# Optimization experiments

Hardware: AMD Instinct MI355X
Metric: run time of the kernel (lower is better)

The kernel has to match this reference:

```python
import jax, jax.numpy as jnp
import numpy as np

K, T, D, S, A, C, H = 128, 64, 128, 512, 4, 16, 512
N_LEAVES = 128
TEMP = 1.0          # sample_merge_temp
EPS_SQRT = 1e-4     # distances.EPSILON ** 0.5 with EPSILON = 1e-8
_SQ_EPS = 1e-12     # numerical guard inside sqrt (diagonal of pairwise dists is 0)


def setup_inputs() -> dict:
    key = jax.random.key(0)
    ks = jax.random.split(key, 11)
    leaf_counts_Kxt = jax.random.randint(ks[0], (K, T), 1, 5)
    embeddings_KxtxD = jax.random.normal(ks[1], (K, T, D), jnp.float32)
    log_felsensteins_KxtxSxA = jax.random.normal(ks[2], (K, T, S, A), jnp.float32)
    site_positions_SxC = jax.random.uniform(ks[3], (S, C), jnp.float32)
    W1 = jax.random.normal(ks[4], (2 * D, H), jnp.float32) / jnp.sqrt(2.0 * D)
    b1 = jnp.zeros((H,), jnp.float32)
    W2 = jax.random.normal(ks[5], (H, D), jnp.float32) / jnp.sqrt(1.0 * H)
    b2 = jnp.zeros((D,), jnp.float32)
    gumbel_Kxtt = jax.random.gumbel(ks[6], (K, T * T), jnp.float32)
    u1_K = jax.random.uniform(ks[7], (K,), jnp.float32, minval=1e-6, maxval=1.0)
    u2_K = jax.random.uniform(ks[8], (K,), jnp.float32, minval=1e-6, maxval=1.0)
    return {
        "N": N_LEAVES,
        "leaf_counts_Kxt": leaf_counts_Kxt,
        "embeddings_KxtxD": embeddings_KxtxD,
        "log_felsensteins_KxtxSxA": log_felsensteins_KxtxSxA,
        "site_positions_SxC": site_positions_SxC,
        "W1": W1, "b1": b1, "W2": W2, "b2": b2,
        "gumbel_Kxtt": gumbel_Kxtt, "u1_K": u1_K, "u2_K": u2_K,
    }


def _merge_encoder(c1_KxD, c2_KxD, W1, b1, W2, b2):
    # MLP merge encoder: MLP(concat(child1, child2)) -> parent embedding
    h = jax.nn.relu(jnp.concatenate([c1_KxD, c2_KxD], axis=-1) @ W1 + b1)
    return h @ W2 + b2


def reference(N, leaf_counts_Kxt, embeddings_KxtxD, log_felsensteins_KxtxSxA,
              site_positions_SxC, W1, b1, W2, b2, gumbel_Kxtt, u1_K, u2_K):
    Kp, t = leaf_counts_Kxt.shape
    ar = jnp.arange(Kp)

    # --- pairwise distances over all t*t subtree pairs per particle ---
    diff_Kxtxtxd = embeddings_KxtxD[:, :, None, :] - embeddings_KxtxD[:, None, :, :]
    pd_Kxtxt = jnp.sqrt(jnp.sum(diff_Kxtxtxd * diff_Kxtxtxd, axis=-1) + _SQ_EPS)
    merge_log_weights_Kxtxt = -pd_Kxtxt / TEMP
    # diagonal_scatter(-inf): forbid self-merges
    eye = jnp.eye(t, dtype=bool)[None]
    merge_log_weights_Kxtxt = jnp.where(eye, -jnp.inf, merge_log_weights_Kxtxt)

    # --- categorical merge sampling (gumbel-max with pre-drawn noise) ---
    flat_Kxtt = merge_log_weights_Kxtxt.reshape(Kp, t * t)
    sample_K = jnp.argmax(flat_Kxtt + gumbel_Kxtt, axis=1)
    idx1_K = sample_K // t
    idx2_K = sample_K % t
    log_merge_prob_K = (flat_Kxtt[ar, sample_K] + jnp.log(2.0)
                        - jax.scipy.special.logsumexp(flat_Kxtt, axis=1))

    # --- merged embedding ---
    child1_KxD = embeddings_KxtxD[ar, idx1_K]
    child2_KxD = embeddings_KxtxD[ar, idx2_K]
    embedding_KxD = _merge_encoder(child1_KxD, child2_KxD, W1, b1, W2, b2)

    # --- branch lengths sampled from Exp(rate = 1/(dist + eps)) ---
    d1_K = jnp.sqrt(jnp.sum((child1_KxD - embedding_KxD) ** 2, axis=-1) + _SQ_EPS)
    d2_K = jnp.sqrt(jnp.sum((child2_KxD - embedding_KxD) ** 2, axis=-1) + _SQ_EPS)
    rate1_K = 1.0 / (d1_K + EPS_SQRT)
    rate2_K = 1.0 / (d2_K + EPS_SQRT)
    branch1_K = -(1.0 / rate1_K) * jnp.log(u1_K)
    branch2_K = -(1.0 / rate2_K) * jnp.log(u2_K)
    log_branch1_prior_K = jnp.log(rate1_K) - rate1_K * branch1_K
    log_branch2_prior_K = jnp.log(rate2_K) - rate2_K * branch2_K

    log_v_plus_K = log_merge_prob_K + log_branch1_prior_K + log_branch2_prior_K

    # --- over-counting correction ---
    ones_K = jnp.sum(leaf_counts_Kxt == 1, axis=1)
    ones_K = ones_K - (leaf_counts_Kxt[ar, idx1_K] == 1).astype(ones_K.dtype)
    ones_K = ones_K - (leaf_counts_Kxt[ar, idx2_K] == 1).astype(ones_K.dtype)
    log_v_minus_K = jnp.log((N - ones_K).astype(jnp.float32))

    return (idx1_K, idx2_K, branch1_K, branch2_K, embedding_KxD,
            log_v_plus_K, log_v_minus_K)
```

## Files before the change

kernel.cpp:

```cpp
#include <hip/hip_runtime.h>
#include <math.h>

#define Kp 128
#define Tn 64
#define Dn 128
#define Hn 512
#define RS 136

typedef __attribute__((ext_vector_type(8))) short short8;
typedef __attribute__((ext_vector_type(4))) float f32x4;

__device__ __forceinline__ float bfpair(unsigned int hi_bits, unsigned int lo_bits) {
    return __uint_as_float(hi_bits) + __uint_as_float(lo_bits);
}

__global__ __launch_bounds__(512, 1) void ep_kernel(
    const int*   __restrict__ Nptr,
    const int*   __restrict__ leaf,
    const float* __restrict__ emb,
    const float* __restrict__ W1,
    const float* __restrict__ b1,
    const float* __restrict__ W2,
    const float* __restrict__ b2,
    const float* __restrict__ gum,
    const float* __restrict__ u1,
    const float* __restrict__ u2,
    float* __restrict__ out)
{
    const int k    = blockIdx.x;
    const int tid  = threadIdx.x;
    const int lane = tid & 63;
    const int wid  = tid >> 6;

    __shared__ unsigned short EH[Tn * RS];
    __shared__ unsigned short EL[Tn * RS];
    __shared__ float hsh[Hn];
    __shared__ float buf[2112];
    __shared__ float nI[Tn];
    __shared__ float sBest[8]; __shared__ int sIdx[8]; __shared__ float sW[8];
    __shared__ float sSum[8];
    __shared__ float sD1[2]; __shared__ float sD2[2];
    __shared__ int   sLeaf[Tn];
    __shared__ int   sOnes;

    const bool gw   = (wid < 4);
    const int itp   = (wid >> 1) & 1;
    const int jtp   = wid & 1;
    const int lrow  = lane & 15;
    const int lq    = lane >> 4;

    const int j0  = 4 * (tid & 127);
    const int ih  = tid >> 7;
    const int ib  = ih * 64;
    const float* W1r = W1 + j0;
    const int jh  = tid >> 5;
    const int jb  = jh * 32;
    const int dd4 = 4 * (tid & 31);

    if (tid < 64) {
        int lc = leaf[k * Tn + tid];
        sLeaf[tid] = lc;
        unsigned long long m = __ballot(lc == 1);
        if (tid == 0) sOnes = __popcll(m);
    }

    float4 ev[4];
    {
        const float4* src = (const float4*)(emb + (size_t)k * Tn * Dn);
        #pragma unroll
        for (int it = 0; it < 4; ++it) ev[it] = src[tid + it * 512];
    }
    float gv[16];
    if (gw) {
        const float* gk = gum + (size_t)k * (Tn * Tn);
        #pragma unroll
        for (int a = 0; a < 2; ++a)
            #pragma unroll
            for (int b = 0; b < 2; ++b) {
                int it = 2 * itp + a, jt = 2 * jtp + b;
                int col = jt * 16 + lrow;
                #pragma unroll
                for (int r = 0; r < 4; ++r) {
                    int row = it * 16 + lq * 4 + r;
                    gv[(a * 2 + b) * 4 + r] = gk[row * Tn + col];
                }
            }
    }
    float b1v = b1[tid];
    float b2v = (tid < 128) ? b2[tid] : 0.0f;
    float u1v = 0.0f, u2v = 0.0f; int Nv = 0;
    if (tid == 0) { u1v = u1[k]; u2v = u2[k]; Nv = Nptr[0]; }

    #pragma unroll
    for (int it = 0; it < 4; ++it) {
        int f4 = tid + it * 512;
        int i  = f4 >> 5;
        int d0 = (f4 & 31) << 2;
        float4 v = ev[it];
        unsigned short hx = __float_as_uint(v.x) >> 16, hy = __float_as_uint(v.y) >> 16,
                       hz = __float_as_uint(v.z) >> 16, hw = __float_as_uint(v.w) >> 16;
        float rx = v.x - __uint_as_float((unsigned int)hx << 16);
        float ry = v.y - __uint_as_float((unsigned int)hy << 16);
        float rz = v.z - __uint_as_float((unsigned int)hz << 16);
        float rw = v.w - __uint_as_float((unsigned int)hw << 16);
        unsigned short lx = __float_as_uint(rx) >> 16, ly = __float_as_uint(ry) >> 16,
                       lz = __float_as_uint(rz) >> 16, lw = __float_as_uint(rw) >> 16;
        *(ushort4*)&EH[i * RS + d0] = make_ushort4(hx, hy, hz, hw);
        *(ushort4*)&EL[i * RS + d0] = make_ushort4(lx, ly, lz, lw);
        float s = v.x * v.x + v.y * v.y + v.z * v.z + v.w * v.w;
        s += __shfl_down(s, 16, 32);
        s += __shfl_down(s,  8, 32);
        s += __shfl_down(s,  4, 32);
        s += __shfl_down(s,  2, 32);
        s += __shfl_down(s,  1, 32);
        if ((lane & 31) == 0) nI[i] = s;
    }
    __syncthreads();

    float4 w1p[16];
    #pragma unroll
    for (int p = 0; p < 16; ++p) w1p[p] = *(const float4*)&W1r[(size_t)(ib + p) * Hn];
    float4 w2p[8];
    #pragma unroll
    for (int p = 0; p < 8; ++p)  w2p[p] = *(const float4*)&W2[(size_t)(jb + p) * Dn + dd4];
    __builtin_amdgcn_sched_barrier(0);

    f32x4 acc[2][2] = {};
    if (gw) {
        const int ka = lq * 8;
        #pragma unroll
        for (int ks = 0; ks < 4; ++ks) {
            int kb  = ks * 32 + ka;
            int ra0 = ((2 * itp + 0) * 16 + lrow) * RS + kb;
            int ra1 = ra0 + 16 * RS;
            int rb0 = ((2 * jtp + 0) * 16 + lrow) * RS + kb;
            int rb1 = rb0 + 16 * RS;
            short8 ah0 = *(const short8*)&EH[ra0], ah1 = *(const short8*)&EH[ra1];
            short8 al0 = *(const short8*)&EL[ra0], al1 = *(const short8*)&EL[ra1];
            short8 bh0 = *(const short8*)&EH[rb0], bh1 = *(const short8*)&EH[rb1];
            short8 bl0 = *(const short8*)&EL[rb0], bl1 = *(const short8*)&EL[rb1];
            acc[0][0] = __builtin_amdgcn_mfma_f32_16x16x32_bf16(ah0, bh0, acc[0][0], 0, 0, 0);
            acc[0][1] = __builtin_amdgcn_mfma_f32_16x16x32_bf16(ah0, bh1, acc[0][1], 0, 0, 0);
            acc[1][0] = __builtin_amdgcn_mfma_f32_16x16x32_bf16(ah1, bh0, acc[1][0], 0, 0, 0);
            acc[1][1] = __builtin_amdgcn_mfma_f32_16x16x32_bf16(ah1, bh1, acc[1][1], 0, 0, 0);
            acc[0][0] = __builtin_amdgcn_mfma_f32_16x16x32_bf16(ah0, bl0, acc[0][0], 0, 0, 0);
            acc[0][1] = __builtin_amdgcn_mfma_f32_16x16x32_bf16(ah0, bl1, acc[0][1], 0, 0, 0);
            acc[1][0] = __builtin_amdgcn_mfma_f32_16x16x32_bf16(ah1, bl0, acc[1][0], 0, 0, 0);
            acc[1][1] = __builtin_amdgcn_mfma_f32_16x16x32_bf16(ah1, bl1, acc[1][1], 0, 0, 0);
            acc[0][0] = __builtin_amdgcn_mfma_f32_16x16x32_bf16(al0, bh0, acc[0][0], 0, 0, 0);
            acc[0][1] = __builtin_amdgcn_mfma_f32_16x16x32_bf16(al0, bh1, acc[0][1], 0, 0, 0);
            acc[1][0] = __builtin_amdgcn_mfma_f32_16x16x32_bf16(al1, bh0, acc[1][0], 0, 0, 0);
            acc[1][1] = __builtin_amdgcn_mfma_f32_16x16x32_bf16(al1, bh1, acc[1][1], 0, 0, 0);
        }
    }

    float es = 0.0f, best = -INFINITY, bestW = 0.0f;
    int   bestIdx = 0;
    if (gw) {
        #pragma unroll
        for (int a = 0; a < 2; ++a)
            #pragma unroll
            for (int b = 0; b < 2; ++b) {
                int it = 2 * itp + a, jt = 2 * jtp + b;
                int col = jt * 16 + lrow;
                float njc = nI[col];
                f32x4 v = acc[a][b];
                float gvals[4] = {v.x, v.y, v.z, v.w};
                #pragma unroll
                for (int r = 0; r < 4; ++r) {
                    int row = it * 16 + lq * 4 + r;
                    float pd2 = nI[row] + njc - 2.0f * gvals[r];
                    pd2 = fmaxf(pd2, 0.0f) + 1e-12f;
                    float wv = (row == col) ? -INFINITY : -sqrtf(pd2);
                    es += expf(wv);
                    float wg = wv + gv[(a * 2 + b) * 4 + r];
                    int idx = row * Tn + col;
                    if (wg > best || (wg == best && idx < bestIdx)) {
                        best = wg; bestIdx = idx; bestW = wv;
                    }
                }
            }
    }
    #pragma unroll
    for (int off = 32; off > 0; off >>= 1) {
        float ob = __shfl_down(best, off);
        int   oi = __shfl_down(bestIdx, off);
        float ow = __shfl_down(bestW, off);
        float oe = __shfl_down(es, off);
        if (ob > best || (ob == best && oi < bestIdx)) { best = ob; bestIdx = oi; bestW = ow; }
        es += oe;
    }
    if (lane == 0) { sBest[wid] = best; sIdx[wid] = bestIdx; sW[wid] = bestW; sSum[wid] = es; }
    __syncthreads();

    float gBest = sBest[0], gW = sW[0], essum = sSum[0];
    int   gIdx = sIdx[0];
    #pragma unroll
    for (int q = 1; q < 8; ++q) {
        float bq = sBest[q]; int iq = sIdx[q];
        if (bq > gBest || (bq == gBest && iq < gIdx)) { gBest = bq; gIdx = iq; gW = sW[q]; }
        essum += sSum[q];
    }
    const int i1 = gIdx >> 6;
    const int i2 = gIdx & 63;

    {
        const int ii    = (ih < 2) ? i1 : i2;
        const int dbase = (ih & 1) * 64;
        const unsigned short* ehr = &EH[ii * RS + dbase];
        const unsigned short* elr = &EL[ii * RS + dbase];
        float4 a = {0, 0, 0, 0};
        #pragma unroll
        for (int r = 0; r < 16; r += 4) {
            uint2 hu = *(const uint2*)&ehr[r];
            uint2 lu = *(const uint2*)&elr[r];
            float x0 = bfpair(hu.x << 16,          lu.x << 16);
            float x1 = bfpair(hu.x & 0xFFFF0000u,  lu.x & 0xFFFF0000u);
            float x2 = bfpair(hu.y << 16,          lu.y << 16);
            float x3 = bfpair(hu.y & 0xFFFF0000u,  lu.y & 0xFFFF0000u);
            float4 w0 = w1p[r + 0], w1 = w1p[r + 1], w2 = w1p[r + 2], w3 = w1p[r + 3];
            a.x += x0 * w0.x + x1 * w1.x + x2 * w2.x + x3 * w3.x;
            a.y += x0 * w0.y + x1 * w1.y + x2 * w2.y + x3 * w3.y;
            a.z += x0 * w0.z + x1 * w1.z + x2 * w2.z + x3 * w3.z;
            a.w += x0 * w0.w + x1 * w1.w + x2 * w2.w + x3 * w3.w;
        }
        #pragma unroll 4
        for (int r = 16; r < 64; r += 4) {
            uint2 hu = *(const uint2*)&ehr[r];
            uint2 lu = *(const uint2*)&elr[r];
            float x0 = bfpair(hu.x << 16,          lu.x << 16);
            float x1 = bfpair(hu.x & 0xFFFF0000u,  lu.x & 0xFFFF0000u);
            float x2 = bfpair(hu.y << 16,          lu.y << 16);
            float x3 = bfpair(hu.y & 0xFFFF0000u,  lu.y & 0xFFFF0000u);
            float4 w0 = *(const float4*)&W1r[(size_t)(ib + r + 0) * Hn];
            float4 w1 = *(const float4*)&W1r[(size_t)(ib + r + 1) * Hn];
            float4 w2 = *(const float4*)&W1r[(size_t)(ib + r + 2) * Hn];
            float4 w3 = *(const float4*)&W1r[(size_t)(ib + r + 3) * Hn];
            a.x += x0 * w0.x + x1 * w1.x + x2 * w2.x + x3 * w3.x;
            a.y += x0 * w0.y + x1 * w1.y + x2 * w2.y + x3 * w3.y;
            a.z += x0 * w0.z + x1 * w1.z + x2 * w2.z + x3 * w3.z;
            a.w += x0 * w0.w + x1 * w1.w + x2 * w2.w + x3 * w3.w;
        }
        *(float4*)&buf[ih * 516 + j0] = a;
    }
    __syncthreads();
    hsh[tid] = fmaxf(b1v + buf[tid] + buf[516 + tid]
                     + buf[1032 + tid] + buf[1548 + tid], 0.0f);
    __syncthreads();

    {
        float4 a = {0, 0, 0, 0};
        #pragma unroll
        for (int j = 0; j < 8; j += 4) {
            float4 h4 = *(const float4*)&hsh[jb + j];
            float4 w0 = w2p[j + 0], w1 = w2p[j + 1], w2 = w2p[j + 2], w3 = w2p[j + 3];
            a.x += h4.x * w0.x + h4.y * w1.x + h4.z * w2.x + h4.w * w3.x;
            a.y += h4.x * w0.y + h4.y * w1.y + h4.z * w2.y + h4.w * w3.y;
            a.z += h4.x * w0.z + h4.y * w1.z + h4.z * w2.z + h4.w * w3.z;
            a.w += h4.x * w0.w + h4.y * w1.w + h4.z * w2.w + h4.w * w3.w;
        }
        #pragma unroll 4
        for (int j = 8; j < 32; j += 4) {
            float4 h4 = *(const float4*)&hsh[jb + j];
            float4 w0 = *(const float4*)&W2[(size_t)(jb + j + 0) * Dn + dd4];
            float4 w1 = *(const float4*)&W2[(size_t)(jb + j + 1) * Dn + dd4];
            float4 w2 = *(const float4*)&W2[(size_t)(jb + j + 2) * Dn + dd4];
            float4 w3 = *(const float4*)&W2[(size_t)(jb + j + 3) * Dn + dd4];
            a.x += h4.x * w0.x + h4.y * w1.x + h4.z * w2.x + h4.w * w3.x;
            a.y += h4.x * w0.y + h4.y * w1.y + h4.z * w2.y + h4.w * w3.y;
            a.z += h4.x * w0.z + h4.y * w1.z + h4.z * w2.z + h4.w * w3.z;
            a.w += h4.x * w0.w + h4.y * w1.w + h4.z * w2.w + h4.w * w3.w;
        }
        *(float4*)&buf[jh * 132 + dd4] = a;
    }
    __syncthreads();

    if (tid < 128) {
        float e = b2v;
        #pragma unroll
        for (int p = 0; p < 16; ++p) e += buf[p * 132 + tid];
        out[4 * Kp + k * Dn + tid] = e;
        float x1d = bfpair((unsigned int)EH[i1 * RS + tid] << 16,
                           (unsigned int)EL[i1 * RS + tid] << 16);
        float x2d = bfpair((unsigned int)EH[i2 * RS + tid] << 16,
                           (unsigned int)EL[i2 * RS + tid] << 16);
        float v1 = (x1d - e) * (x1d - e);
        float v2 = (x2d - e) * (x2d - e);
        #pragma unroll
        for (int off = 32; off > 0; off >>= 1) {
            v1 += __shfl_down(v1, off);
            v2 += __shfl_down(v2, off);
        }
        if (lane == 0) { sD1[wid] = v1; sD2[wid] = v2; }
    }
    __syncthreads();

    if (tid == 0) {
        float s1 = sD1[0] + sD1[1];
        float s2 = sD2[0] + sD2[1];
        float d1 = sqrtf(s1 + 1e-12f);
        float d2 = sqrtf(s2 + 1e-12f);
        float rate1 = 1.0f / (d1 + 1e-4f);
        float rate2 = 1.0f / (d2 + 1e-4f);
        float branch1 = -(1.0f / rate1) * logf(u1v);
        float branch2 = -(1.0f / rate2) * logf(u2v);
        float lbp1 = logf(rate1) - rate1 * branch1;
        float lbp2 = logf(rate2) - rate2 * branch2;
        float lse  = logf(essum);
        float lmp  = gW + 0.69314718055994531f - lse;
        float lvp  = lmp + lbp1 + lbp2;
        int ones = sOnes - (sLeaf[i1] == 1 ? 1 : 0) - (sLeaf[i2] == 1 ? 1 : 0);
        float lvm = logf((float)(Nv - ones));

        out[k]                         = (float)i1;
        out[Kp + k]                    = (float)i2;
        out[2 * Kp + k]                = branch1;
        out[3 * Kp + k]                = branch2;
        out[4 * Kp + Kp * Dn + k]      = lvp;
        out[4 * Kp + Kp * Dn + Kp + k] = lvm;
    }
}

extern "C" void kernel_launch(void* const* d_in, const int* in_sizes, int n_in,
                              void* d_out, int out_size, void* d_ws, size_t ws_size,
                              hipStream_t stream) {
    const int*   Nptr = (const int*)  d_in[0];
    const int*   leaf = (const int*)  d_in[1];
    const float* emb  = (const float*)d_in[2];
    const float* W1   = (const float*)d_in[5];
    const float* b1   = (const float*)d_in[6];
    const float* W2   = (const float*)d_in[7];
    const float* b2   = (const float*)d_in[8];
    const float* gum  = (const float*)d_in[9];
    const float* u1   = (const float*)d_in[10];
    const float* u2   = (const float*)d_in[11];
    float* out = (float*)d_out;

    ep_kernel<<<Kp, 512, 0, stream>>>(Nptr, leaf, emb, W1, b1, W2, b2, gum, u1, u2, out);
}
```

Before: 127.5 us.

## Drop register-prefetched weights and rotate MLP weight row order per block

Removes the early register prefetch of the first W1/W2 rows that overlapped with the distance MFMA phase. All weight rows are now streamed from global memory, starting each block's loop at a row offset derived from the particle index. The rotation is meant to spread concurrent blocks across different weight rows and cut cache or channel contention, and dropping the prefetch frees registers. The cost is that weight-load latency is no longer hidden behind the pairwise-distance compute, and floating-point summation order now varies per block.

```diff
diff --git a/kernel.cpp b/kernel.cpp
--- a/kernel.cpp
+++ b/kernel.cpp
@@ -56,6 +56,9 @@
     const int jh  = tid >> 5;
     const int jb  = jh * 32;
     const int dd4 = 4 * (tid & 31);
+
+    const int rot1 = ((k >> 3) & 15) << 2;
+    const int rot2 = ((k >> 3) & 7)  << 2;
 
     if (tid < 64) {
         int lc = leaf[k * Tn + tid];
@@ -117,14 +120,6 @@
     }
     __syncthreads();
 
-    float4 w1p[16];
-    #pragma unroll
-    for (int p = 0; p < 16; ++p) w1p[p] = *(const float4*)&W1r[(size_t)(ib + p) * Hn];
-    float4 w2p[8];
-    #pragma unroll
-    for (int p = 0; p < 8; ++p)  w2p[p] = *(const float4*)&W2[(size_t)(jb + p) * Dn + dd4];
-    __builtin_amdgcn_sched_barrier(0);
-
     f32x4 acc[2][2] = {};
     if (gw) {
         const int ka = lq * 8;
@@ -210,22 +205,9 @@
         const unsigned short* ehr = &EH[ii * RS + dbase];
         const unsigned short* elr = &EL[ii * RS + dbase];
         float4 a = {0, 0, 0, 0};
-        #pragma unroll
-        for (int r = 0; r < 16; r += 4) {
-            uint2 hu = *(const uint2*)&ehr[r];
-            uint2 lu = *(const uint2*)&elr[r];
-            float x0 = bfpair(hu.x << 16,          lu.x << 16);
-            float x1 = bfpair(hu.x & 0xFFFF0000u,  lu.x & 0xFFFF0000u);
-            float x2 = bfpair(hu.y << 16,          lu.y << 16);
-            float x3 = bfpair(hu.y & 0xFFFF0000u,  lu.y & 0xFFFF0000u);
-            float4 w0 = w1p[r + 0], w1 = w1p[r + 1], w2 = w1p[r + 2], w3 = w1p[r + 3];
-            a.x += x0 * w0.x + x1 * w1.x + x2 * w2.x + x3 * w3.x;
-            a.y += x0 * w0.y + x1 * w1.y + x2 * w2.y + x3 * w3.y;
-            a.z += x0 * w0.z + x1 * w1.z + x2 * w2.z + x3 * w3.z;
-            a.w += x0 * w0.w + x1 * w1.w + x2 * w2.w + x3 * w3.w;
-        }
         #pragma unroll 4
-        for (int r = 16; r < 64; r += 4) {
+        for (int s = 0; s < 64; s += 4) {
+            int r = (rot1 + s) & 63;
             uint2 hu = *(const uint2*)&ehr[r];
             uint2 lu = *(const uint2*)&elr[r];
             float x0 = bfpair(hu.x << 16,          lu.x << 16);
@@ -250,17 +232,9 @@
 
     {
         float4 a = {0, 0, 0, 0};
-        #pragma unroll
-        for (int j = 0; j < 8; j += 4) {
-            float4 h4 = *(const float4*)&hsh[jb + j];
-            float4 w0 = w2p[j + 0], w1 = w2p[j + 1], w2 = w2p[j + 2], w3 = w2p[j + 3];
-            a.x += h4.x * w0.x + h4.y * w1.x + h4.z * w2.x + h4.w * w3.x;
-            a.y += h4.x * w0.y + h4.y * w1.y + h4.z * w2.y + h4.w * w3.y;
-            a.z += h4.x * w0.z + h4.y * w1.z + h4.z * w2.z + h4.w * w3.z;
-            a.w += h4.x * w0.w + h4.y * w1.w + h4.z * w2.w + h4.w * w3.w;
-        }
         #pragma unroll 4
-        for (int j = 8; j < 32; j += 4) {
+        for (int s = 0; s < 32; s += 4) {
+            int j = (rot2 + s) & 31;
             float4 h4 = *(const float4*)&hsh[jb + j];
             float4 w0 = *(const float4*)&W2[(size_t)(jb + j + 0) * Dn + dd4];
             float4 w1 = *(const float4*)&W2[(size_t)(jb + j + 1) * Dn + dd4];
```

Result: no change. 125.3 us (-1.7%).
